# Kernel optimization log

Hardware: AMD Instinct MI355X
Metric: run time of the kernel (lower is better)

Reference implementation:

```python
import jax, jax.numpy as jnp
import numpy as np
import math

ALPHA = 0.6
BETA = 0.4
NPTS = 1000   # trapezoid points, matches beta_cdf default npts
EPS = 1e-10   # lower integration limit, matches zeros(...) + 1e-10
# log Beta(alpha, beta) normalizer
BETALN = math.lgamma(ALPHA) + math.lgamma(BETA) - math.lgamma(ALPHA + BETA)


def beta_logpdf(x):
    # torch.distributions.Beta(ALPHA, BETA).log_prob(x)
    return (ALPHA - 1.0) * jnp.log(x) + (BETA - 1.0) * jnp.log1p(-x) - BETALN


def setup_inputs() -> dict:
    key = jax.random.key(0)
    # probabilities in (0,1); uniform like a sigmoid-gate output
    x = jax.random.uniform(key, (512, 128), dtype=jnp.float32)
    return {"x": x}


def reference(x):
    n, c = x.shape
    sorted_x = jnp.sort(x, axis=0)                                  # [n, c]
    # linspace grid from EPS to each sorted value: [NPTS, n, c]
    steps = (jnp.arange(NPTS, dtype=x.dtype) / (NPTS - 1))[:, None, None]
    grid = EPS + steps * (sorted_x - EPS)
    pdf = jnp.exp(beta_logpdf(grid))                                # [NPTS, n, c]
    # replicate torch's check: skip first point if pdf(EPS) > 1
    # (static: depends only on the fixed alpha/beta constants)
    pdf0 = math.exp((ALPHA - 1.0) * math.log(EPS)
                    + (BETA - 1.0) * math.log1p(-EPS) - BETALN)
    start = 1 if pdf0 > 1.0 else 0
    g = grid[start:]
    p = pdf[start:]
    # trapezoidal rule along the integration axis -> pcdf [n, c]
    pcdf = 0.5 * jnp.sum((p[1:] + p[:-1]) * (g[1:] - g[:-1]), axis=0)
    ecdf = (jnp.arange(1, n + 1, dtype=x.dtype) / (n + 1))[:, None]  # [n, 1]
    # sum of squared CDF gaps over all columns, divided by n
    loss = jnp.sum((pcdf - ecdf) ** 2) / n
    return loss
```

## Files before the change

### kernel.cpp

```cpp
#include <hip/hip_runtime.h>
#include <cmath>

#define N_ROWS 512
#define N_COLS 128

__device__ __forceinline__ float betacf(float a, float b, float x) {
    float qab = a + b, qap = a + 1.0f, qam = a - 1.0f;
    float c = 1.0f;
    float d = 1.0f - qab * x / qap;
    if (fabsf(d) < 1e-30f) d = 1e-30f;
    d = 1.0f / d;
    float h = d;
    #pragma unroll
    for (int m = 1; m <= 16; ++m) {
        float fm = (float)m, m2 = 2.0f * fm;
        float aa = fm * (b - fm) * x / ((qam + m2) * (a + m2));
        d = 1.0f + aa * d; if (fabsf(d) < 1e-30f) d = 1e-30f;
        c = 1.0f + aa / c; if (fabsf(c) < 1e-30f) c = 1e-30f;
        d = 1.0f / d;
        h *= d * c;
        aa = -(a + fm) * (qab + fm) * x / ((a + m2) * (qap + m2));
        d = 1.0f + aa * d; if (fabsf(d) < 1e-30f) d = 1e-30f;
        c = 1.0f + aa / c; if (fabsf(c) < 1e-30f) c = 1e-30f;
        d = 1.0f / d;
        h *= d * c;
    }
    return h;
}

__global__ __launch_bounds__(512) void sort_loss(const float* __restrict__ x,
                                                 float* __restrict__ partials,
                                                 float lnB, float invB, float c_head) {
    __shared__ float sd[N_ROWS];
    const int tid = threadIdx.x;
    const int col = blockIdx.x;
    float v = x[tid * N_COLS + col];
    for (int k = 2; k <= N_ROWS; k <<= 1) {
        for (int j = k >> 1; j > 0; j >>= 1) {
            float pv;
            if (j >= 64) {
                __syncthreads();
                sd[tid] = v;
                __syncthreads();
                pv = sd[tid ^ j];
            } else {
                pv = __shfl_xor(v, j, 64);
            }
            const bool lower = (tid & j) == 0;
            const bool asc   = (tid & k) == 0;
            v = (lower == asc) ? fminf(v, pv) : fmaxf(v, pv);
        }
    }
    const float s  = fmaxf(v, 1e-30f);
    const float sm = s - 1e-10f;
    const float h  = sm * (1.0f / 999.0f);
    const float x1 = 1e-10f + h;

    const float ls  = __logf(s);
    const float om  = fmaxf(1.0f - s, 1e-30f);
    const float lom = __logf(om);
    const float bt  = __expf(fmaf(0.6f, ls, fmaf(0.4f, lom, -lnB)));
    float I;
    if (s < 0.53333333f)
        I = bt * betacf(0.6f, 0.4f, s) * (1.0f / 0.6f);
    else
        I = 1.0f - bt * betacf(0.4f, 0.6f, om) * (1.0f / 0.4f);

    const float head = c_head * __expf(0.6f * __logf(x1));

    const float sm04 = __expf(-0.4f * ls);
    float wp      = om;
    float wp_m06  = __expf(-0.6f * __logf(wp));
    float wp_p04  = wp * wp_m06;
    float dr = 0.0f;
    #pragma unroll
    for (int j = 1; j <= 8; ++j) {
        float w    = fmaf((float)j, h, om);
        float wm06 = __expf(-0.6f * __logf(w));
        float wp04 = w * wm06;
        float trap = 0.5f * h * (wp_m06 + wm06);
        float ex   = (wp04 - wp_p04) * 2.5f;
        dr += trap - ex;
        wp_m06 = wm06; wp_p04 = wp04;
    }
    dr *= sm04 * invB;

    const float T    = I - head + dr;
    const float ecdf = (float)(tid + 1) * (1.0f / 513.0f);
    const float d    = T - ecdf;
    float val = d * d;

    #pragma unroll
    for (int off = 32; off > 0; off >>= 1)
        val += __shfl_down(val, off);
    __syncthreads();
    if ((tid & 63) == 0) sd[tid >> 6] = val;
    __syncthreads();
    if (tid == 0) {
        float bs = 0.0f;
        #pragma unroll
        for (int w = 0; w < 8; ++w) bs += sd[w];
        partials[col] = bs;
    }
}

__global__ __launch_bounds__(64) void reduce_partials(const float* __restrict__ partials,
                                                      float* __restrict__ out) {
    float acc = partials[threadIdx.x] + partials[threadIdx.x + 64];
    #pragma unroll
    for (int off = 32; off > 0; off >>= 1)
        acc += __shfl_down(acc, off);
    if (threadIdx.x == 0)
        out[0] = acc * (1.0f / (float)N_ROWS);
}

extern "C" void kernel_launch(void* const* d_in, const int* in_sizes, int n_in,
                              void* d_out, int out_size, void* d_ws, size_t ws_size,
                              hipStream_t stream) {
    const float* x = (const float*)d_in[0];
    float* out = (float*)d_out;
    float* partials = (float*)d_ws;

    const double B = exp(lgamma(0.6) + lgamma(0.4) - lgamma(1.0));
    const float lnB    = (float)log(B);
    const float invB   = (float)(1.0 / B);
    const float c_head = (float)(1.0 / (0.6 * B) - 0.03185 / B);

    sort_loss<<<N_COLS, N_ROWS, 0, stream>>>(x, partials, lnB, invB, c_head);
    reduce_partials<<<1, 64, 0, stream>>>(partials, out);
}
```

Before: 67.77 us.

## Replace bitonic sort with per-element rank counting across split blocks

The per-column bitonic sort, with its many barrier-separated shared-memory stages, is replaced by a rank count: each thread counts how many column entries are smaller than its value (ties broken by index) and uses that rank for the empirical CDF. The loss sum does not depend on order, so the sorted array is never built. Each column is now split across two 256-thread blocks, giving 256 blocks instead of 128, and the partial reduction reads 256 partials. Each thread now does O(n) shared-memory comparisons instead of the log-squared sort stages.

```diff
diff --git a/kernel.cpp b/kernel.cpp
--- a/kernel.cpp
+++ b/kernel.cpp
@@ -28,29 +28,34 @@
     return h;
 }
 
-__global__ __launch_bounds__(512) void sort_loss(const float* __restrict__ x,
-                                                 float* __restrict__ partials,
-                                                 float lnB, float invB, float c_head) {
-    __shared__ float sd[N_ROWS];
+__global__ __launch_bounds__(256, 1) void rank_loss(const float* __restrict__ x,
+                                                    float* __restrict__ partials,
+                                                    float lnB, float invB, float c_head) {
+    __shared__ float col[N_ROWS];
+    __shared__ float swave[4];
     const int tid = threadIdx.x;
-    const int col = blockIdx.x;
-    float v = x[tid * N_COLS + col];
-    for (int k = 2; k <= N_ROWS; k <<= 1) {
-        for (int j = k >> 1; j > 0; j >>= 1) {
-            float pv;
-            if (j >= 64) {
-                __syncthreads();
-                sd[tid] = v;
-                __syncthreads();
-                pv = sd[tid ^ j];
-            } else {
-                pv = __shfl_xor(v, j, 64);
-            }
-            const bool lower = (tid & j) == 0;
-            const bool asc   = (tid & k) == 0;
-            v = (lower == asc) ? fminf(v, pv) : fmaxf(v, pv);
-        }
+    const int b   = blockIdx.x;
+    const int c   = b >> 1;
+    const int r   = ((b & 1) << 8) + tid;
+
+    col[tid]       = x[tid * N_COLS + c];
+    col[tid + 256] = x[(tid + 256) * N_COLS + c];
+    __syncthreads();
+
+    const float v = col[r];
+
+    int cnt = 0;
+    const float4* col4 = (const float4*)col;
+    #pragma unroll 8
+    for (int i4 = 0; i4 < N_ROWS / 4; ++i4) {
+        const float4 q = col4[i4];
+        const int base = i4 << 2;
+        cnt += (q.x < v) || ((q.x == v) && (base     < r));
+        cnt += (q.y < v) || ((q.y == v) && (base + 1 < r));
+        cnt += (q.z < v) || ((q.z == v) && (base + 2 < r));
+        cnt += (q.w < v) || ((q.w == v) && (base + 3 < r));
     }
+
     const float s  = fmaxf(v, 1e-30f);
     const float sm = s - 1e-10f;
     const float h  = sm * (1.0f / 999.0f);
@@ -86,31 +91,27 @@
     dr *= sm04 * invB;
 
     const float T    = I - head + dr;
-    const float ecdf = (float)(tid + 1) * (1.0f / 513.0f);
+    const float ecdf = (float)(cnt + 1) * (1.0f / 513.0f);
     const float d    = T - ecdf;
     float val = d * d;
 
     #pragma unroll
     for (int off = 32; off > 0; off >>= 1)
         val += __shfl_down(val, off);
+    if ((tid & 63) == 0) swave[tid >> 6] = val;
     __syncthreads();
-    if ((tid & 63) == 0) sd[tid >> 6] = val;
-    __syncthreads();
-    if (tid == 0) {
-        float bs = 0.0f;
-        #pragma unroll
-        for (int w = 0; w < 8; ++w) bs += sd[w];
-        partials[col] = bs;
-    }
+    if (tid == 0)
+        partials[b] = swave[0] + swave[1] + swave[2] + swave[3];
 }
 
 __global__ __launch_bounds__(64) void reduce_partials(const float* __restrict__ partials,
                                                       float* __restrict__ out) {
-    float acc = partials[threadIdx.x] + partials[threadIdx.x + 64];
+    const int tid = threadIdx.x;
+    float acc = partials[tid] + partials[tid + 64] + partials[tid + 128] + partials[tid + 192];
     #pragma unroll
     for (int off = 32; off > 0; off >>= 1)
         acc += __shfl_down(acc, off);
-    if (threadIdx.x == 0)
+    if (tid == 0)
         out[0] = acc * (1.0f / (float)N_ROWS);
 }
 
@@ -126,6 +127,6 @@
     const float invB   = (float)(1.0 / B);
     const float c_head = (float)(1.0 / (0.6 * B) - 0.03185 / B);
 
-    sort_loss<<<N_COLS, N_ROWS, 0, stream>>>(x, partials, lnB, invB, c_head);
+    rank_loss<<<2 * N_COLS, 256, 0, stream>>>(x, partials, lnB, invB, c_head);
     reduce_partials<<<1, 64, 0, stream>>>(partials, out);
 }
```

New measurement: 75.80 us. 11.8% more time.
